# Kernel optimization log

Hardware: AMD Instinct MI355X
Metric: run time of the kernel (lower is better)

The kernel has to match this reference:

```python
import jax, jax.numpy as jnp
import numpy as np

EPS = 1e-5
K_NUM, EDGE_TYPE = 5, 2  # k_num = A_fixed_partitions(3) + edge_type(2)


def _bn(x, gamma, beta):
    # training-mode BatchNorm2d: batch stats over (N, T, V) per channel
    m = jnp.mean(x, axis=(0, 2, 3), keepdims=True)
    v = jnp.var(x, axis=(0, 2, 3), keepdims=True)
    return (x - m) * jax.lax.rsqrt(v + EPS) * gamma[None, :, None, None] + beta[None, :, None, None]


def setup_inputs() -> dict:
    key = jax.random.key(0)
    ks = jax.random.split(key, 6)
    N, C, T, V = 32, 64, 300, 25
    Cout, Kt = 64, 9
    x = jax.random.normal(ks[0], (N, C, T, V), jnp.float32)
    A = jax.random.uniform(ks[1], (K_NUM - EDGE_TYPE, V, V), jnp.float32) / V  # fixed adjacency (already scaled by edge_importance)
    B = jax.random.uniform(ks[2], (N, EDGE_TYPE, V, V), jnp.float32) / V      # per-sample adaptive adjacency A_act
    lamda_act = jnp.full((1,), 0.5, jnp.float32)
    conv_w = jax.random.normal(ks[3], (Cout * K_NUM, C), jnp.float32) * (1.0 / np.sqrt(C))  # 1x1 conv weight
    conv_b = jnp.zeros((Cout * K_NUM,), jnp.float32)
    bn1_g = jnp.ones((Cout,), jnp.float32)
    bn1_b = jnp.zeros((Cout,), jnp.float32)
    tcn_w = jax.random.normal(ks[4], (Cout, Cout, Kt, 1), jnp.float32) * (1.0 / np.sqrt(Cout * Kt))
    tcn_b = jnp.zeros((Cout,), jnp.float32)
    bn2_g = jnp.ones((Cout,), jnp.float32)
    bn2_b = jnp.zeros((Cout,), jnp.float32)
    return dict(x=x, A=A, B=B, lamda_act=lamda_act, conv_w=conv_w, conv_b=conv_b,
                bn1_g=bn1_g, bn1_b=bn1_b, tcn_w=tcn_w, tcn_b=tcn_b, bn2_g=bn2_g, bn2_b=bn2_b)


def reference(x, A, B, lamda_act, conv_w, conv_b, bn1_g, bn1_b, tcn_w, tcn_b, bn2_g, bn2_b):
    n, c, t, v = x.shape
    res = x  # identity residual (in_ch == out_ch, stride 1)
    # SpatialGcn: 1x1 conv (pure channel GEMM) -> split -> dual einsum graph conv
    y = jnp.einsum('nctv,oc->notv', x, conv_w) + conv_b[None, :, None, None]  # (n, K*Cout, t, v)
    cout = y.shape[1] // K_NUM
    y = y.reshape(n, K_NUM, cout, t, v)
    x1 = jnp.einsum('nkctv,kvw->nctw', y[:, :K_NUM - EDGE_TYPE], A)   # fixed adjacency
    x2 = jnp.einsum('nkctv,nkvw->nctw', y[:, K_NUM - EDGE_TYPE:], B)  # adaptive adjacency
    g = x1 + x2 * lamda_act[0]
    # tcn: BN -> ReLU -> temporal conv (9,1) pad (4,0) -> BN -> Dropout(0)=identity
    h = jax.nn.relu(_bn(g, bn1_g, bn1_b))
    h = jax.lax.conv_general_dilated(h, tcn_w, window_strides=(1, 1),
                                     padding=((4, 4), (0, 0)),
                                     dimension_numbers=('NCHW', 'OIHW', 'NCHW'))
    h = h + tcn_b[None, :, None, None]
    h = _bn(h, bn2_g, bn2_b)
    return jax.nn.relu(h + res)
```

## Files before the change

### kernel.cpp

```cpp
#include <hip/hip_runtime.h>
#include <hip/hip_bf16.h>

#define N_  32
#define C_  64
#define T_  300
#define V_  25
#define TV  (T_*V_)
#define CTV (C_*TV)
#define NELEM (N_*CTV)
#define CNTF 240000.0f
#define PROWS 7788

typedef float f32x4 __attribute__((ext_vector_type(4)));
typedef short bf16x8 __attribute__((ext_vector_type(8)));
typedef short s4v __attribute__((ext_vector_type(4)));
typedef short s8v __attribute__((ext_vector_type(8)));

__device__ __forceinline__ unsigned short f2bf(float f) {
    unsigned u = __float_as_uint(f);
    unsigned r = u + 0x7fffu + ((u >> 16) & 1u);
    return (unsigned short)(r >> 16);
}
__device__ __forceinline__ float bf2f(unsigned short u) {
    return __uint_as_float(((unsigned)u) << 16);
}
__device__ __forceinline__ unsigned cvt_pk(float lo, float hi) {
    unsigned r;
    asm("v_cvt_pk_bf16_f32 %0, %1, %2" : "=v"(r) : "v"(lo), "v"(hi));
    return r;
}

__global__ __launch_bounds__(256) void k_prep(
    const float* __restrict__ conv_w, const float* __restrict__ tw,
    const float* __restrict__ A,
    unsigned short* __restrict__ w2b, unsigned short* __restrict__ twb,
    unsigned short* __restrict__ ashA)
{
    int tid = blockIdx.x*256 + threadIdx.x;
    for (int e = tid; e < 20480; e += 8192) {
        int ks = e >> 11, c = (e >> 5) & 63, kk = e & 31;
        w2b[e] = f2bf(conv_w[(((ks>>1)*64 + c)*64) + (ks&1)*32 + kk]);
    }
    for (int e = tid; e < 36864; e += 8192) {
        int gi = e >> 11, c = (e >> 5) & 63, kk = e & 31;
        int dt = gi >> 1, ks = gi & 1;
        twb[e] = f2bf(tw[(c*64 + 32*ks + kk)*9 + dt]);
    }
    for (int e = tid; e < 3840; e += 8192) {
        int k = e / 1280, r = e - k*1280, w = r / 40, v = r % 40;
        float val = (w < 25 && v < 25) ? A[k*625 + v*25 + w] : 0.f;
        ashA[e] = f2bf(val);
    }
}

__global__ __launch_bounds__(256) void k_prepn(
    const float* __restrict__ A, const float* __restrict__ B,
    const float* __restrict__ lamda,
    unsigned short* __restrict__ bshB, float* __restrict__ csumN)
{
    const int n = blockIdx.x, tid = threadIdx.x;
    const float lam = lamda[0];
    unsigned short* dst = bshB + n*2560;
    {
        s8v z8 = {0,0,0,0,0,0,0,0};
        for (int e = tid; e < 320; e += 256) *(s8v*)&dst[e*8] = z8;
    }
    __syncthreads();
    for (int e = tid; e < 1250; e += 256) {
        int k = e / 625, r = e - k*625, v = r / 25, w = r - v*25;
        dst[k*1280 + w*40 + v] = f2bf(lam * B[((n<<1) + k)*625 + r]);
    }
    for (int e = tid; e < 160; e += 256) {
        int k = e / 32, w = e % 32;
        float s = 0.f;
        if (w < 25) {
            if (k < 3) { for (int v = 0; v < 25; ++v) s += bf2f(f2bf(A[k*625 + v*25 + w])); }
            else       { for (int v = 0; v < 25; ++v) s += bf2f(f2bf(lam * B[((n<<1)+(k-3))*625 + v*25 + w])); }
        }
        csumN[n*160 + e] = s;
    }
}

__global__ __launch_bounds__(256) void k_gcn(
    const float* __restrict__ x,
    const unsigned short* __restrict__ ashA, const unsigned short* __restrict__ bshB,
    const float* __restrict__ csumN,
    const unsigned short* __restrict__ w2b, const float* __restrict__ conv_b,
    unsigned short* __restrict__ gout, float* __restrict__ stats3)
{
    __shared__ unsigned short ash[6400];
    __shared__ unsigned short zsh[10496];

    const int tb = blockIdx.x, n = blockIdx.y;
    const int t0 = tb*5;
    const int tid = threadIdx.x;
    const int lane = tid & 63, wv = tid >> 6;
    const int lg = lane >> 4, lr = lane & 15;
    const int crow = lr + 16*wv;
    const int cbase = 16*wv + 4*lg;

    bf16x8 wfrag[10];
    #pragma unroll
    for (int ks = 0; ks < 10; ++ks)
        wfrag[ks] = *(const bf16x8*)&w2b[(ks*64 + crow)*32 + 8*lg];

    for (int e = tid; e < 480; e += 256)
        *(s8v*)&ash[e*8] = *(const s8v*)&ashA[e*8];
    for (int e = tid; e < 320; e += 256)
        *(s8v*)&ash[3840 + e*8] = *(const s8v*)&bshB[n*2560 + e*8];

    const float* csum = csumN + n*160;
    float bs0[4], bs1[4];
    #pragma unroll
    for (int r = 0; r < 4; ++r) {
        float s0 = 0.f, s1 = 0.f;
        #pragma unroll
        for (int k = 0; k < 5; ++k) {
            float cb = conv_b[k*64 + cbase + r];
            s0 += cb * csum[k*32 + lr];
            s1 += cb * csum[k*32 + lr + 16];
        }
        bs0[r] = s0; bs1[r] = s1;
    }

    float sacc[4] = {0,0,0,0}, qacc[4] = {0,0,0,0};

    const float* xrow = x + n*CTV + crow*TV + t0*V_;
    float xf[8];
    #pragma unroll
    for (int i = 0; i < 8; ++i) { int v = 8*lg + i; xf[i] = (v < 25) ? xrow[v] : 0.f; }

    __syncthreads();

    for (int tl = 0; tl < 5; ++tl) {
        union { bf16x8 v; unsigned u[4]; } xu;
        #pragma unroll
        for (int p = 0; p < 4; ++p) xu.u[p] = cvt_pk(xf[2*p], xf[2*p+1]);
        bf16x8 xfrag = xu.v;
        if (tl < 4) {
            const float* xn = xrow + (tl+1)*V_;
            #pragma unroll
            for (int i = 0; i < 8; ++i) { int v = 8*lg + i; xf[i] = (v < 25) ? xn[v] : 0.f; }
        }
        #pragma unroll
        for (int k = 0; k < 5; ++k)
        #pragma unroll
        for (int nt = 0; nt < 2; ++nt) {
            bf16x8 bfrag = *(const bf16x8*)&ash[k*1280 + (lr + 16*nt)*40 + 8*lg];
            f32x4 z = {0.f,0.f,0.f,0.f};
            z = __builtin_amdgcn_mfma_f32_16x16x32_bf16(xfrag, bfrag, z, 0, 0, 0);
            uint2 zz;
            zz.x = cvt_pk(z[0], z[1]);
            zz.y = cvt_pk(z[2], z[3]);
            *(uint2*)&zsh[(lr + 16*nt)*328 + k*64 + 16*wv + 4*lg] = zz;
        }
        __syncthreads();
        f32x4 acc0 = {0.f,0.f,0.f,0.f}, acc1 = {0.f,0.f,0.f,0.f};
        #pragma unroll
        for (int ks = 0; ks < 10; ++ks) {
            bf16x8 b0 = *(const bf16x8*)&zsh[lr*328 + 32*ks + 8*lg];
            bf16x8 b1 = *(const bf16x8*)&zsh[(lr+16)*328 + 32*ks + 8*lg];
            acc0 = __builtin_amdgcn_mfma_f32_16x16x32_bf16(wfrag[ks], b0, acc0, 0, 0, 0);
            acc1 = __builtin_amdgcn_mfma_f32_16x16x32_bf16(wfrag[ks], b1, acc1, 0, 0, 0);
        }
        float v0a[4], v1a[4];
        #pragma unroll
        for (int r = 0; r < 4; ++r) {
            v0a[r] = acc0[r] + bs0[r];
            v1a[r] = acc1[r] + bs1[r];
            sacc[r] += v0a[r] + (lr < 9 ? v1a[r] : 0.f);
            qacc[r] += v0a[r]*v0a[r] + (lr < 9 ? v1a[r]*v1a[r] : 0.f);
        }
        unsigned short* grow = gout + (size_t)(n*300 + t0 + tl)*1600;
        uint2 g0, g1;
        g0.x = cvt_pk(v0a[0], v0a[1]); g0.y = cvt_pk(v0a[2], v0a[3]);
        g1.x = cvt_pk(v1a[0], v1a[1]); g1.y = cvt_pk(v1a[2], v1a[3]);
        *(uint2*)&grow[lr*64 + cbase] = g0;
        if (lr < 9) *(uint2*)&grow[(lr+16)*64 + cbase] = g1;
        __syncthreads();
    }

    #pragma unroll
    for (int r = 0; r < 4; ++r) {
        float s = sacc[r], q = qacc[r];
        s += __shfl_xor(s, 1); s += __shfl_xor(s, 2);
        s += __shfl_xor(s, 4); s += __shfl_xor(s, 8);
        q += __shfl_xor(q, 1); q += __shfl_xor(q, 2);
        q += __shfl_xor(q, 4); q += __shfl_xor(q, 8);
        if (lr == 0) {
            stats3[(n*60 + tb)*128 + cbase + r] = s;
            stats3[(n*60 + tb)*128 + 64 + cbase + r] = q;
        }
    }
}

__global__ __launch_bounds__(256) void k_fin(
    const float* __restrict__ src, int count, float* __restrict__ sbo,
    const float* __restrict__ gma, const float* __restrict__ bta)
{
    const int c = blockIdx.x, tid = threadIdx.x;
    float s = 0.f, q = 0.f;
    for (int b = tid; b < count; b += 256) {
        s += src[b*128 + c];
        q += src[b*128 + 64 + c];
    }
    #pragma unroll
    for (int m = 1; m < 64; m <<= 1) { s += __shfl_xor(s, m); q += __shfl_xor(q, m); }
    __shared__ float rs[4], rq[4];
    if ((tid & 63) == 0) { rs[tid>>6] = s; rq[tid>>6] = q; }
    __syncthreads();
    if (tid == 0) {
        s = rs[0]+rs[1]+rs[2]+rs[3]; q = rq[0]+rq[1]+rq[2]+rq[3];
        float mean = s / CNTF, var = q / CNTF - mean*mean;
        float sc = gma[c] * rsqrtf(var + 1e-5f);
        sbo[c] = sc;
        sbo[64 + c] = bta[c] - mean*sc;
    }
}

__global__ __launch_bounds__(256) void k_bn1(
    const unsigned short* __restrict__ g, const float* __restrict__ sb,
    unsigned short* __restrict__ p)
{
    __shared__ float sbs[128];
    if (threadIdx.x < 128) sbs[threadIdx.x] = sb[threadIdx.x];
    __syncthreads();
    int idx = blockIdx.x*256 + threadIdx.x;
    int n = idx / (PROWS*8);
    int rem = idx - n*(PROWS*8);
    int row = (rem >> 3) - 128;
    int q8 = (rem & 7) * 8;
    uint4 out4 = {0,0,0,0};
    if (row >= 0 && row < 7500) {
        s8v raw = *(const s8v*)&g[((size_t)n*7500 + row)*64 + q8];
        float f[8];
        #pragma unroll
        for (int j = 0; j < 8; ++j)
            f[j] = fmaxf(fmaf(bf2f((unsigned short)raw[j]), sbs[q8+j], sbs[64+q8+j]), 0.f);
        out4.x = cvt_pk(f[0], f[1]); out4.y = cvt_pk(f[2], f[3]);
        out4.z = cvt_pk(f[4], f[5]); out4.w = cvt_pk(f[6], f[7]);
    }
    *(uint4*)&p[(size_t)idx*8] = out4;
}

__global__ __launch_bounds__(256) void k_tcn(
    const unsigned short* __restrict__ p, const unsigned short* __restrict__ twb,
    const float* __restrict__ tb, unsigned short* __restrict__ hout,
    float* __restrict__ stats4)
{
    __shared__ unsigned short lds[328*64];

    const int bj = blockIdx.x, n = blockIdx.y;
    const int j0 = bj*128;
    const int tid = threadIdx.x;
    const int lane = tid & 63, ct = tid >> 6;
    const int lg = lane >> 4, lr = lane & 15;
    const int cA = ct*16 + lr;
    const int cbase = ct*16 + 4*lg;

    const unsigned short* psrc = p + ((size_t)n*PROWS + 28 + j0)*64;
    for (int e = tid; e < 2624; e += 256) {
        int row = e >> 3, q = e & 7;
        s8v v = *(const s8v*)&psrc[(size_t)row*64 + q*8];
        *(s8v*)&lds[row*64 + ((q ^ (row & 7)))*8] = v;
    }

    f32x4 acc[8];
    #pragma unroll
    for (int i = 0; i < 8; ++i) acc[i] = (f32x4){0.f,0.f,0.f,0.f};
    float tbc[4];
    #pragma unroll
    for (int r = 0; r < 4; ++r) tbc[r] = tb[cbase + r];

    __syncthreads();

    #pragma unroll
    for (int ks = 0; ks < 2; ++ks) {
        bf16x8 af[9];
        #pragma unroll
        for (int dt = 0; dt < 9; ++dt)
            af[dt] = *(const bf16x8*)&twb[((2*dt + ks)*64 + cA)*32 + 8*lg];
        #pragma unroll
        for (int jt = 0; jt < 8; ++jt) {
            #pragma unroll
            for (int dt = 0; dt < 9; ++dt) {
                int row = 16*jt + lr + 25*dt;
                bf16x8 b = *(const bf16x8*)&lds[row*64 + ((4*ks + lg) ^ (row & 7))*8];
                acc[jt] = __builtin_amdgcn_mfma_f32_16x16x32_bf16(af[dt], b, acc[jt], 0, 0, 0);
            }
        }
    }

    float sacc[4] = {0,0,0,0}, qacc[4] = {0,0,0,0};
    #pragma unroll
    for (int jt = 0; jt < 8; ++jt) {
        int j = j0 + 16*jt + lr;
        if (j < 7500) {
            #pragma unroll
            for (int r = 0; r < 4; ++r) {
                float v = acc[jt][r] + tbc[r];
                sacc[r] += v; qacc[r] += v*v;
            }
        }
    }
    #pragma unroll
    for (int r = 0; r < 4; ++r) {
        float s = sacc[r], q = qacc[r];
        s += __shfl_xor(s, 1); s += __shfl_xor(s, 2);
        s += __shfl_xor(s, 4); s += __shfl_xor(s, 8);
        q += __shfl_xor(q, 1); q += __shfl_xor(q, 2);
        q += __shfl_xor(q, 4); q += __shfl_xor(q, 8);
        if (lr == 0) {
            float* dst = stats4 + (size_t)(n*59 + bj)*128;
            dst[cbase + r] = s;
            dst[64 + cbase + r] = q;
        }
    }

    __syncthreads();
    #pragma unroll
    for (int jt = 0; jt < 8; ++jt)
        #pragma unroll
        for (int r = 0; r < 4; ++r)
            lds[(cbase + r)*136 + 16*jt + lr] = f2bf(acc[jt][r] + tbc[r]);
    __syncthreads();
    for (int e = tid; e < 2048; e += 256) {
        int row = e >> 5, c4 = (e & 31) << 2;
        int j = j0 + c4;
        if (j < 7500)
            *(s4v*)&hout[(size_t)(n*64 + row)*7500 + j] = *(const s4v*)&lds[row*136 + c4];
    }
}

__global__ __launch_bounds__(256) void k_out(
    const unsigned short* __restrict__ h, const float* __restrict__ x,
    const float* __restrict__ sb, float* __restrict__ out)
{
    int i4 = blockIdx.x * 256 + threadIdx.x;
    if (i4 >= NELEM/4) return;
    int c = ((i4*4) / TV) & 63;
    float s2 = sb[128 + c], b2 = sb[192 + c];
    s4v hv = *(const s4v*)&h[i4*4];
    float4 xv = ((const float4*)x)[i4];
    float4 o;
    o.x = fmaxf(fmaf(bf2f((unsigned short)hv[0]), s2, b2) + xv.x, 0.f);
    o.y = fmaxf(fmaf(bf2f((unsigned short)hv[1]), s2, b2) + xv.y, 0.f);
    o.z = fmaxf(fmaf(bf2f((unsigned short)hv[2]), s2, b2) + xv.z, 0.f);
    o.w = fmaxf(fmaf(bf2f((unsigned short)hv[3]), s2, b2) + xv.w, 0.f);
    ((float4*)out)[i4] = o;
}

extern "C" void kernel_launch(void* const* d_in, const int* in_sizes, int n_in,
                              void* d_out, int out_size, void* d_ws, size_t ws_size,
                              hipStream_t stream)
{
    const float* x      = (const float*)d_in[0];
    const float* A      = (const float*)d_in[1];
    const float* B      = (const float*)d_in[2];
    const float* lamda  = (const float*)d_in[3];
    const float* conv_w = (const float*)d_in[4];
    const float* conv_b = (const float*)d_in[5];
    const float* bn1_g  = (const float*)d_in[6];
    const float* bn1_b  = (const float*)d_in[7];
    const float* tcn_w  = (const float*)d_in[8];
    const float* tcn_b  = (const float*)d_in[9];
    const float* bn2_g  = (const float*)d_in[10];
    const float* bn2_b  = (const float*)d_in[11];

    unsigned short* g = (unsigned short*)d_ws;
    unsigned short* p = g + NELEM;
    unsigned short* h = p + (size_t)N_*PROWS*64;
    float* stats3 = (float*)(h + NELEM);
    float* stats4 = stats3 + 1920*128;
    float* sb     = stats4 + 1888*128;
    float* csumN  = sb + 256;
    unsigned short* w2b  = (unsigned short*)(csumN + 32*160);
    unsigned short* twb  = w2b + 20480;
    unsigned short* ashA = twb + 36864;
    unsigned short* bshB = ashA + 3840;

    k_prep<<<32, 256, 0, stream>>>(conv_w, tcn_w, A, w2b, twb, ashA);
    k_prepn<<<32, 256, 0, stream>>>(A, B, lamda, bshB, csumN);
    k_gcn<<<dim3(60, N_), 256, 0, stream>>>(x, ashA, bshB, csumN, w2b, conv_b, g, stats3);
    k_fin<<<64, 256, 0, stream>>>(stats3, 1920, sb, bn1_g, bn1_b);
    k_bn1<<<PROWS, 256, 0, stream>>>(g, sb, p);
    k_tcn<<<dim3(59, N_), 256, 0, stream>>>(p, twb, tcn_b, h, stats4);
    k_fin<<<64, 256, 0, stream>>>(stats4, 1888, sb + 128, bn2_g, bn2_b);
    k_out<<<NELEM/4/256, 256, 0, stream>>>(h, x, sb, (float*)d_out);
}
```

Before: 139.7 us.

## Fuse BN1+ReLU into temporal conv load and read adjacency from global

Removes the separate k_bn1 pass and its padded intermediate buffer p. k_tcn now loads g directly, applies the BN1 scale/shift and ReLU while staging into LDS, and zero-fills rows outside the valid time range. Separately, k_gcn drops its LDS copy of the adjacency fragments and the barrier after it, reading B fragments straight from global/L2 inside the MFMA loop. This saves a full write and read of the intermediate tensor and one launch, but adds ALU work to the tcn staging and may add global-load latency in the gcn inner loop.

```diff
diff --git a/kernel.cpp b/kernel.cpp
--- a/kernel.cpp
+++ b/kernel.cpp
@@ -9,7 +9,6 @@
 #define CTV (C_*TV)
 #define NELEM (N_*CTV)
 #define CNTF 240000.0f
-#define PROWS 7788
 
 typedef float f32x4 __attribute__((ext_vector_type(4)));
 typedef short bf16x8 __attribute__((ext_vector_type(8)));
@@ -88,7 +87,6 @@
     const unsigned short* __restrict__ w2b, const float* __restrict__ conv_b,
     unsigned short* __restrict__ gout, float* __restrict__ stats3)
 {
-    __shared__ unsigned short ash[6400];
     __shared__ unsigned short zsh[10496];
 
     const int tb = blockIdx.x, n = blockIdx.y;
@@ -104,11 +102,6 @@
     for (int ks = 0; ks < 10; ++ks)
         wfrag[ks] = *(const bf16x8*)&w2b[(ks*64 + crow)*32 + 8*lg];
 
-    for (int e = tid; e < 480; e += 256)
-        *(s8v*)&ash[e*8] = *(const s8v*)&ashA[e*8];
-    for (int e = tid; e < 320; e += 256)
-        *(s8v*)&ash[3840 + e*8] = *(const s8v*)&bshB[n*2560 + e*8];
-
     const float* csum = csumN + n*160;
     float bs0[4], bs1[4];
     #pragma unroll
@@ -129,8 +122,6 @@
     float xf[8];
     #pragma unroll
     for (int i = 0; i < 8; ++i) { int v = 8*lg + i; xf[i] = (v < 25) ? xrow[v] : 0.f; }
-
-    __syncthreads();
 
     for (int tl = 0; tl < 5; ++tl) {
         union { bf16x8 v; unsigned u[4]; } xu;
@@ -146,7 +137,9 @@
         for (int k = 0; k < 5; ++k)
         #pragma unroll
         for (int nt = 0; nt < 2; ++nt) {
-            bf16x8 bfrag = *(const bf16x8*)&ash[k*1280 + (lr + 16*nt)*40 + 8*lg];
+            const unsigned short* asrc = (k < 3) ? (ashA + k*1280)
+                                                 : (bshB + n*2560 + (k-3)*1280);
+            bf16x8 bfrag = *(const bf16x8*)&asrc[(lr + 16*nt)*40 + 8*lg];
             f32x4 z = {0.f,0.f,0.f,0.f};
             z = __builtin_amdgcn_mfma_f32_16x16x32_bf16(xfrag, bfrag, z, 0, 0, 0);
             uint2 zz;
@@ -218,37 +211,13 @@
     }
 }
 
-__global__ __launch_bounds__(256) void k_bn1(
+__global__ __launch_bounds__(256) void k_tcn(
     const unsigned short* __restrict__ g, const float* __restrict__ sb,
-    unsigned short* __restrict__ p)
-{
+    const unsigned short* __restrict__ twb, const float* __restrict__ tb,
+    unsigned short* __restrict__ hout, float* __restrict__ stats4)
+{
+    __shared__ unsigned short lds[328*64];
     __shared__ float sbs[128];
-    if (threadIdx.x < 128) sbs[threadIdx.x] = sb[threadIdx.x];
-    __syncthreads();
-    int idx = blockIdx.x*256 + threadIdx.x;
-    int n = idx / (PROWS*8);
-    int rem = idx - n*(PROWS*8);
-    int row = (rem >> 3) - 128;
-    int q8 = (rem & 7) * 8;
-    uint4 out4 = {0,0,0,0};
-    if (row >= 0 && row < 7500) {
-        s8v raw = *(const s8v*)&g[((size_t)n*7500 + row)*64 + q8];
-        float f[8];
-        #pragma unroll
-        for (int j = 0; j < 8; ++j)
-            f[j] = fmaxf(fmaf(bf2f((unsigned short)raw[j]), sbs[q8+j], sbs[64+q8+j]), 0.f);
-        out4.x = cvt_pk(f[0], f[1]); out4.y = cvt_pk(f[2], f[3]);
-        out4.z = cvt_pk(f[4], f[5]); out4.w = cvt_pk(f[6], f[7]);
-    }
-    *(uint4*)&p[(size_t)idx*8] = out4;
-}
-
-__global__ __launch_bounds__(256) void k_tcn(
-    const unsigned short* __restrict__ p, const unsigned short* __restrict__ twb,
-    const float* __restrict__ tb, unsigned short* __restrict__ hout,
-    float* __restrict__ stats4)
-{
-    __shared__ unsigned short lds[328*64];
 
     const int bj = blockIdx.x, n = blockIdx.y;
     const int j0 = bj*128;
@@ -258,11 +227,25 @@
     const int cA = ct*16 + lr;
     const int cbase = ct*16 + 4*lg;
 
-    const unsigned short* psrc = p + ((size_t)n*PROWS + 28 + j0)*64;
+    if (tid < 128) sbs[tid] = sb[tid];
+    __syncthreads();
+
     for (int e = tid; e < 2624; e += 256) {
         int row = e >> 3, q = e & 7;
-        s8v v = *(const s8v*)&psrc[(size_t)row*64 + q*8];
-        *(s8v*)&lds[row*64 + ((q ^ (row & 7)))*8] = v;
+        int gr = j0 - 100 + row;
+        uint4 pk4 = {0,0,0,0};
+        if (gr >= 0 && gr < 7500) {
+            s8v raw = *(const s8v*)&g[((size_t)n*7500 + gr)*64 + q*8];
+            float f[8];
+            #pragma unroll
+            for (int j = 0; j < 8; ++j)
+                f[j] = fmaxf(fmaf(bf2f((unsigned short)raw[j]), sbs[q*8+j], sbs[64+q*8+j]), 0.f);
+            pk4.x = cvt_pk(f[0], f[1]);
+            pk4.y = cvt_pk(f[2], f[3]);
+            pk4.z = cvt_pk(f[4], f[5]);
+            pk4.w = cvt_pk(f[6], f[7]);
+        }
+        *(uint4*)&lds[row*64 + ((q ^ (row & 7)))*8] = pk4;
     }
 
     f32x4 acc[8];
@@ -368,8 +351,7 @@
     const float* bn2_b  = (const float*)d_in[11];
 
     unsigned short* g = (unsigned short*)d_ws;
-    unsigned short* p = g + NELEM;
-    unsigned short* h = p + (size_t)N_*PROWS*64;
+    unsigned short* h = g + NELEM;
     float* stats3 = (float*)(h + NELEM);
     float* stats4 = stats3 + 1920*128;
     float* sb     = stats4 + 1888*128;
@@ -383,8 +365,7 @@
     k_prepn<<<32, 256, 0, stream>>>(A, B, lamda, bshB, csumN);
     k_gcn<<<dim3(60, N_), 256, 0, stream>>>(x, ashA, bshB, csumN, w2b, conv_b, g, stats3);
     k_fin<<<64, 256, 0, stream>>>(stats3, 1920, sb, bn1_g, bn1_b);
-    k_bn1<<<PROWS, 256, 0, stream>>>(g, sb, p);
-    k_tcn<<<dim3(59, N_), 256, 0, stream>>>(p, twb, tcn_b, h, stats4);
+    k_tcn<<<dim3(59, N_), 256, 0, stream>>>(g, sb, twb, tcn_b, h, stats4);
     k_fin<<<64, 256, 0, stream>>>(stats4, 1888, sb + 128, bn2_g, bn2_b);
     k_out<<<NELEM/4/256, 256, 0, stream>>>(h, x, sb, (float*)d_out);
 }
```

Measured after the change: 144.3 us. +3.3%, slower.
